# Kernel optimization log

Measured on AMD Instinct MI355X. Metric: run time of the kernel, lower is better.

## Reference

```python
import jax, jax.numpy as jnp
import numpy as np

TEMPERATURE = 0.2
EPS = 1e-8
N, D = 8192, 256
EDGE_PROB = 0.002  # ~16 neighbors per node


def setup_inputs() -> dict:
    key = jax.random.key(0)
    k1, k2, k3 = jax.random.split(key, 3)
    z_view = jax.random.normal(k1, (N, D), dtype=jnp.float32)
    z_fused = jax.random.normal(k2, (N, D), dtype=jnp.float32)
    # sparse binary fused-graph adjacency, densified (matches Gf_sparse.to_dense())
    Gf_dense = (jax.random.uniform(k3, (N, N)) < EDGE_PROB).astype(jnp.float32)
    return {"z_view": z_view, "z_fused": z_fused, "Gf_dense": Gf_dense}


def _l2_normalize(x, eps=1e-12):
    # matches F.normalize(p=2, dim=1): x / max(||x||, eps)
    norm = jnp.sqrt(jnp.sum(x * x, axis=1, keepdims=True))
    return x / jnp.maximum(norm, eps)


def reference(z_view, z_fused, Gf_dense):
    n = z_view.shape[0]
    zv = _l2_normalize(z_view)
    zf = _l2_normalize(z_fused)
    sim = jnp.matmul(zv, zf.T) / TEMPERATURE  # [N, N]
    eye = jnp.eye(n, dtype=sim.dtype)
    pos_mask = ((eye + Gf_dense) > 0).astype(sim.dtype)  # diag always 1
    neg_mask = 1.0 - pos_mask
    pos_scores = jnp.sum(sim * pos_mask, axis=1, keepdims=True) / (
        jnp.sum(pos_mask, axis=1, keepdims=True) + EPS
    )  # [N, 1]
    neg_scores = sim * neg_mask  # [N, N] (positive slots zeroed, kept as logits)
    logits = jnp.concatenate([pos_scores, neg_scores], axis=1)  # [N, N+1]
    # CrossEntropyLoss(reduction='sum') with labels == 0, then / N
    lse = jax.nn.logsumexp(logits, axis=1)
    loss = jnp.sum(lse - logits[:, 0]) / n
    return loss
```

## Files before the change

### kernel.cpp

```cpp
#include <hip/hip_runtime.h>

#define NROW 8192
#define DIM  256
#define INV_T 5.0f
#define BM 128
#define BN 128
#define CSPLIT 8
#define COLS_PER_BLOCK (NROW / CSPLIT)
#define NT (COLS_PER_BLOCK / BN)
#define TOTAL_STEPS (NT * (DIM / 32))

typedef _Float16 f16x8 __attribute__((ext_vector_type(8)));
typedef _Float16 f16x4 __attribute__((ext_vector_type(4)));
typedef float    f32x4 __attribute__((ext_vector_type(4)));

__device__ __forceinline__ void gload_lds16(const void* g, void* l) {
  __builtin_amdgcn_global_load_lds(
      (__attribute__((address_space(1))) void*)(g),
      (__attribute__((address_space(3))) void*)(l),
      16, 0, 0);
}

__global__ __launch_bounds__(256) void norm_kernel(
    const float* __restrict__ zv, const float* __restrict__ zf,
    _Float16* __restrict__ ov, _Float16* __restrict__ of) {
  const float* in  = blockIdx.y ? zf : zv;
  _Float16*    out = blockIdx.y ? of : ov;
  int row  = blockIdx.x * 4 + (threadIdx.x >> 6);
  int lane = threadIdx.x & 63;
  float4 v = ((const float4*)(in + (size_t)row * DIM))[lane];
  float ss = v.x * v.x + v.y * v.y + v.z * v.z + v.w * v.w;
#pragma unroll
  for (int off = 1; off < 64; off <<= 1) ss += __shfl_xor(ss, off);
  float inv = 1.0f / fmaxf(sqrtf(ss), 1e-12f);
  f16x4 o;
  o.x = (_Float16)(v.x * inv);
  o.y = (_Float16)(v.y * inv);
  o.z = (_Float16)(v.z * inv);
  o.w = (_Float16)(v.w * inv);
  ((f16x4*)(out + (size_t)row * DIM))[lane] = o;
}

__global__ __launch_bounds__(256, 2) void fused_kernel(
    const _Float16* __restrict__ zv, const _Float16* __restrict__ zf,
    const float* __restrict__ Gf,
    float* __restrict__ Sp, float* __restrict__ Pp, float* __restrict__ Cp) {

  __shared__ __align__(16) _Float16 Asf[BM * DIM];
  __shared__ __align__(16) _Float16 Bs[2][BN * 32];

  const int t    = threadIdx.x;
  const int lane = t & 63;
  const int w    = t >> 6;
  const int wr   = w >> 1;
  const int wc   = w & 1;
  const int l15  = lane & 15;
  const int kq   = lane >> 4;
  const int row0 = blockIdx.x * BM;
  const int col0 = blockIdx.y * COLS_PER_BLOCK;

#pragma unroll
  for (int c = 0; c < 16; ++c) {
    int i = c * 256 + t;
    int row = i >> 5, cbP = i & 31;
    int cbL = cbP ^ (row & 7);
    gload_lds16(zv + (size_t)(row0 + row) * DIM + cbL * 8,
                &Asf[(size_t)(c * 256 + w * 64) * 8]);
  }

  auto stageB = [&](int buf, int s) {
    int tt = s >> 3, kk = s & 7;
    int ct0 = col0 + tt * BN;
    int k0 = kk * 32;
#pragma unroll
    for (int c = 0; c < 2; ++c) {
      int i = c * 256 + t;
      int row = i >> 2, cbP = i & 3;
      int cbL = cbP ^ ((row >> 1) & 3);
      gload_lds16(zf + (size_t)(ct0 + row) * DIM + k0 + cbL * 8,
                  &Bs[buf][(size_t)(c * 256 + w * 64) * 8]);
    }
  };

  stageB(0, 0);
  asm volatile("s_waitcnt vmcnt(0)" ::: "memory");
  __syncthreads();

  f32x4 acc[4][4];
  float Sa[16], Pa[16], Ca[16];
#pragma unroll
  for (int i = 0; i < 16; ++i) { Sa[i] = 0.0f; Pa[i] = 0.0f; Ca[i] = 0.0f; }

#pragma unroll 2
  for (int s = 0; s < TOTAL_STEPS; ++s) {
    const int cur = s & 1;
    if ((s & 7) == 0) {
#pragma unroll
      for (int m = 0; m < 4; ++m)
#pragma unroll
        for (int n = 0; n < 4; ++n) acc[m][n] = (f32x4)(0.0f);
    }
    if (s < TOTAL_STEPS - 1) stageB(cur ^ 1, s + 1);

    const int k0 = (s & 7) * 32;
    f16x8 af[4], bf[4];
#pragma unroll
    for (int m = 0; m < 4; ++m) {
      int row = wr * 64 + m * 16 + l15;
      int cbL = (k0 >> 3) + kq;
      int cbP = cbL ^ (row & 7);
      af[m] = *(const f16x8*)&Asf[(size_t)row * 256 + cbP * 8];
    }
#pragma unroll
    for (int n = 0; n < 4; ++n) {
      int row = wc * 64 + n * 16 + l15;
      int cbP = kq ^ ((row >> 1) & 3);
      bf[n] = *(const f16x8*)&Bs[cur][(size_t)row * 32 + cbP * 8];
    }
#pragma unroll
    for (int m = 0; m < 4; ++m)
#pragma unroll
      for (int n = 0; n < 4; ++n)
        acc[m][n] = __builtin_amdgcn_mfma_f32_16x16x32_f16(af[m], bf[n], acc[m][n], 0, 0, 0);

    if ((s & 7) == 7) {
      int tt = s >> 3;
      int ct0 = col0 + tt * BN;
#pragma unroll
      for (int m = 0; m < 4; ++m) {
        int gi = row0 + wr * 64 + m * 16 + kq * 4;
#pragma unroll
        for (int n = 0; n < 4; ++n) {
          int gj = ct0 + wc * 64 + n * 16 + l15;
          const float* gp = Gf + (size_t)gi * NROW + gj;
#pragma unroll
          for (int r = 0; r < 4; ++r) {
            float sim = acc[m][n][r] * INV_T;
            float g = gp[(size_t)r * NROW];
            bool pos = (g > 0.0f) || ((gi + r) == gj);
            float e = __expf(sim);
            int idx = m * 4 + r;
            Sa[idx] += pos ? 1.0f : e;
            Pa[idx] += pos ? sim : 0.0f;
            Ca[idx] += pos ? 1.0f : 0.0f;
          }
        }
      }
    }
    asm volatile("s_waitcnt vmcnt(0)" ::: "memory");
    __syncthreads();
  }

#pragma unroll
  for (int off = 1; off <= 8; off <<= 1) {
#pragma unroll
    for (int i = 0; i < 16; ++i) {
      Sa[i] += __shfl_xor(Sa[i], off);
      Pa[i] += __shfl_xor(Pa[i], off);
      Ca[i] += __shfl_xor(Ca[i], off);
    }
  }
  const int slot = blockIdx.y * 2 + wc;
#pragma unroll
  for (int i = 0; i < 16; ++i) {
    if (l15 == i) {
      int m = i >> 2, r = i & 3;
      int row = row0 + wr * 64 + m * 16 + kq * 4 + r;
      Sp[(size_t)slot * NROW + row] = Sa[i];
      Pp[(size_t)slot * NROW + row] = Pa[i];
      Cp[(size_t)slot * NROW + row] = Ca[i];
    }
  }
}

__global__ __launch_bounds__(256) void loss_partial_kernel(
    const float* __restrict__ Sp, const float* __restrict__ Pp,
    const float* __restrict__ Cp, float* __restrict__ bsum) {
  int row = blockIdx.x * 256 + threadIdx.x;
  float S = 0.0f, P = 0.0f, C = 0.0f;
#pragma unroll
  for (int s2 = 0; s2 < 16; ++s2) {
    S += Sp[(size_t)s2 * NROW + row];
    P += Pp[(size_t)s2 * NROW + row];
    C += Cp[(size_t)s2 * NROW + row];
  }
  float pos = P / (C + 1e-8f);
  float contrib = __logf(S + __expf(pos)) - pos;
#pragma unroll
  for (int off = 1; off < 64; off <<= 1) contrib += __shfl_xor(contrib, off);
  __shared__ float wsum[4];
  if ((threadIdx.x & 63) == 0) wsum[threadIdx.x >> 6] = contrib;
  __syncthreads();
  if (threadIdx.x == 0) bsum[blockIdx.x] = wsum[0] + wsum[1] + wsum[2] + wsum[3];
}

__global__ void loss_final_kernel(const float* __restrict__ bsum, float* __restrict__ out) {
  int lane = threadIdx.x;
  float v = (lane < 32) ? bsum[lane] : 0.0f;
#pragma unroll
  for (int off = 1; off < 64; off <<= 1) v += __shfl_xor(v, off);
  if (lane == 0) out[0] = v / (float)NROW;
}

extern "C" void kernel_launch(void* const* d_in, const int* in_sizes, int n_in,
                              void* d_out, int out_size, void* d_ws, size_t ws_size,
                              hipStream_t stream) {
  const float* zv = (const float*)d_in[0];
  const float* zf = (const float*)d_in[1];
  const float* Gf = (const float*)d_in[2];
  float* out = (float*)d_out;

  char* ws = (char*)d_ws;
  _Float16* zv16 = (_Float16*)ws;
  _Float16* zf16 = zv16 + (size_t)NROW * DIM;
  float* Sp = (float*)(ws + 2 * (size_t)NROW * DIM * sizeof(_Float16));
  float* Pp = Sp + 16 * (size_t)NROW;
  float* Cp = Pp + 16 * (size_t)NROW;
  float* bsum = Cp + 16 * (size_t)NROW;

  norm_kernel<<<dim3(NROW / 4, 2), 256, 0, stream>>>(zv, zf, zv16, zf16);
  fused_kernel<<<dim3(NROW / BM, CSPLIT), 256, 0, stream>>>(zv16, zf16, Gf, Sp, Pp, Cp);
  loss_partial_kernel<<<NROW / 256, 256, 0, stream>>>(Sp, Pp, Cp, bsum);
  loss_final_kernel<<<1, 64, 0, stream>>>(bsum, out);
}
```

Baseline: 113.4 us.

## Prefetch adjacency tiles as float4 into ballot bitmasks overlapped with MFMA steps

Replaces the per-element scalar Gf loads in the epilogue with vectorized float4 loads of the next column tile's adjacency, issued during the K-steps of the current tile and packed into per-wave 64-bit masks via ballots. The epilogue then tests bits instead of waiting on global loads. The K loop is fully unrolled per tile with fine-grained vmcnt waits and raw s_barrier in place of __syncthreads. This is meant to hide the latency of the scattered Gf reads behind compute, at the cost of more registers and more complex wait-count bookkeeping.

Result: faster. 102.6 us (-9.5%).

```diff
diff --git a/kernel.cpp b/kernel.cpp
--- a/kernel.cpp
+++ b/kernel.cpp
@@ -7,12 +7,12 @@
 #define BN 128
 #define CSPLIT 8
 #define COLS_PER_BLOCK (NROW / CSPLIT)
-#define NT (COLS_PER_BLOCK / BN)
-#define TOTAL_STEPS (NT * (DIM / 32))
+#define NT 8
 
 typedef _Float16 f16x8 __attribute__((ext_vector_type(8)));
 typedef _Float16 f16x4 __attribute__((ext_vector_type(4)));
 typedef float    f32x4 __attribute__((ext_vector_type(4)));
+typedef unsigned long long u64;
 
 __device__ __forceinline__ void gload_lds16(const void* g, void* l) {
   __builtin_amdgcn_global_load_lds(
@@ -49,9 +49,9 @@
   __shared__ __align__(16) _Float16 Asf[BM * DIM];
   __shared__ __align__(16) _Float16 Bs[2][BN * 32];
 
-  const int t    = threadIdx.x;
-  const int lane = t & 63;
-  const int w    = t >> 6;
+  const int t_   = threadIdx.x;
+  const int lane = t_ & 63;
+  const int w    = t_ >> 6;
   const int wr   = w >> 1;
   const int wc   = w & 1;
   const int l15  = lane & 15;
@@ -61,7 +61,7 @@
 
 #pragma unroll
   for (int c = 0; c < 16; ++c) {
-    int i = c * 256 + t;
+    int i = c * 256 + t_;
     int row = i >> 5, cbP = i & 31;
     int cbL = cbP ^ (row & 7);
     gload_lds16(zv + (size_t)(row0 + row) * DIM + cbL * 8,
@@ -74,7 +74,7 @@
     int k0 = kk * 32;
 #pragma unroll
     for (int c = 0; c < 2; ++c) {
-      int i = c * 256 + t;
+      int i = c * 256 + t_;
       int row = i >> 2, cbP = i & 3;
       int cbL = cbP ^ ((row >> 1) & 3);
       gload_lds16(zf + (size_t)(ct0 + row) * DIM + k0 + cbL * 8,
@@ -82,74 +82,126 @@
     }
   };
 
+  auto issueGf = [&](float4* q, int tt, int c0) {
+    const float* base = Gf + (size_t)(row0 + wr * 64 + (lane >> 4)) * NROW
+                           + col0 + tt * BN + wc * 64 + l15 * 4;
+#pragma unroll
+    for (int j = 0; j < 4; ++j)
+      q[j] = *(const float4*)(base + (size_t)((c0 + j) * 4) * NROW);
+  };
+
+  auto maskFrom4 = [&](const float4* q) -> u64 {
+    u64 e = 0;
+#pragma unroll
+    for (int j = 0; j < 4; ++j) {
+      u64 b0 = __ballot(q[j].x > 0.0f);
+      u64 b1 = __ballot(q[j].y > 0.0f);
+      u64 b2 = __ballot(q[j].z > 0.0f);
+      u64 b3 = __ballot(q[j].w > 0.0f);
+      u64 s01 = (l15 & 1) ? b1 : b0;
+      u64 s23 = (l15 & 1) ? b3 : b2;
+      u64 bsel = (l15 & 2) ? s23 : s01;
+      u64 ej = bsel >> (l15 >> 2);
+      e = (kq == j) ? ej : e;
+    }
+    return e;
+  };
+
   stageB(0, 0);
+
+  u64 wm[4];
+  {
+    float4 gp[8];
+#pragma unroll
+    for (int c = 0; c < 8; ++c) issueGf(gp + c, 0, c);
+    wm[0] = maskFrom4(gp);
+    wm[1] = maskFrom4(gp + 4);
+#pragma unroll
+    for (int c = 0; c < 8; ++c) issueGf(gp + c, 0, 8 + c);
+    wm[2] = maskFrom4(gp);
+    wm[3] = maskFrom4(gp + 4);
+  }
   asm volatile("s_waitcnt vmcnt(0)" ::: "memory");
-  __syncthreads();
+  __builtin_amdgcn_s_barrier();
 
   f32x4 acc[4][4];
   float Sa[16], Pa[16], Ca[16];
+  u64 wn[4];
+  float4 gvA[4], gvB[4];
 #pragma unroll
   for (int i = 0; i < 16; ++i) { Sa[i] = 0.0f; Pa[i] = 0.0f; Ca[i] = 0.0f; }
 
-#pragma unroll 2
-  for (int s = 0; s < TOTAL_STEPS; ++s) {
-    const int cur = s & 1;
-    if ((s & 7) == 0) {
-#pragma unroll
-      for (int m = 0; m < 4; ++m)
-#pragma unroll
-        for (int n = 0; n < 4; ++n) acc[m][n] = (f32x4)(0.0f);
-    }
-    if (s < TOTAL_STEPS - 1) stageB(cur ^ 1, s + 1);
-
-    const int k0 = (s & 7) * 32;
-    f16x8 af[4], bf[4];
-#pragma unroll
-    for (int m = 0; m < 4; ++m) {
-      int row = wr * 64 + m * 16 + l15;
-      int cbL = (k0 >> 3) + kq;
-      int cbP = cbL ^ (row & 7);
-      af[m] = *(const f16x8*)&Asf[(size_t)row * 256 + cbP * 8];
-    }
-#pragma unroll
-    for (int n = 0; n < 4; ++n) {
-      int row = wc * 64 + n * 16 + l15;
-      int cbP = kq ^ ((row >> 1) & 3);
-      bf[n] = *(const f16x8*)&Bs[cur][(size_t)row * 32 + cbP * 8];
-    }
-#pragma unroll
-    for (int m = 0; m < 4; ++m)
-#pragma unroll
-      for (int n = 0; n < 4; ++n)
-        acc[m][n] = __builtin_amdgcn_mfma_f32_16x16x32_f16(af[m], bf[n], acc[m][n], 0, 0, 0);
-
-    if ((s & 7) == 7) {
-      int tt = s >> 3;
-      int ct0 = col0 + tt * BN;
-#pragma unroll
-      for (int m = 0; m < 4; ++m) {
-        int gi = row0 + wr * 64 + m * 16 + kq * 4;
-#pragma unroll
-        for (int n = 0; n < 4; ++n) {
-          int gj = ct0 + wc * 64 + n * 16 + l15;
-          const float* gp = Gf + (size_t)gi * NROW + gj;
-#pragma unroll
-          for (int r = 0; r < 4; ++r) {
-            float sim = acc[m][n][r] * INV_T;
-            float g = gp[(size_t)r * NROW];
-            bool pos = (g > 0.0f) || ((gi + r) == gj);
-            float e = __expf(sim);
-            int idx = m * 4 + r;
-            Sa[idx] += pos ? 1.0f : e;
-            Pa[idx] += pos ? sim : 0.0f;
-            Ca[idx] += pos ? 1.0f : 0.0f;
-          }
-        }
-      }
-    }
-    asm volatile("s_waitcnt vmcnt(0)" ::: "memory");
-    __syncthreads();
-  }
+#define STEP(KK)                                                               \
+  do {                                                                         \
+    if ((KK) == 0) {                                                           \
+      _Pragma("unroll") for (int m = 0; m < 4; ++m)                            \
+          _Pragma("unroll") for (int n = 0; n < 4; ++n)                        \
+              acc[m][n] = (f32x4)(0.0f);                                       \
+    }                                                                          \
+    f16x8 af[4], bf[4];                                                        \
+    _Pragma("unroll") for (int m = 0; m < 4; ++m) {                            \
+      int row = wr * 64 + m * 16 + l15;                                        \
+      int cbL = ((KK) * 32 >> 3) + kq;                                         \
+      int cbP = cbL ^ (row & 7);                                               \
+      af[m] = *(const f16x8*)&Asf[(size_t)row * 256 + cbP * 8];                \
+    }                                                                          \
+    _Pragma("unroll") for (int n = 0; n < 4; ++n) {                            \
+      int row = wc * 64 + n * 16 + l15;                                        \
+      int cbP = kq ^ ((row >> 1) & 3);                                         \
+      bf[n] = *(const f16x8*)&Bs[(KK) & 1][(size_t)row * 32 + cbP * 8];        \
+    }                                                                          \
+    if (t < NT - 1 || (KK) < 7) stageB(((KK) + 1) & 1, t * 8 + (KK) + 1);      \
+    asm volatile("" ::: "memory");                                             \
+    if ((KK) < 4) {                                                            \
+      if (t < NT - 1) issueGf(((KK) & 1) ? gvB : gvA, t + 1, (KK) * 4);        \
+    }                                                                          \
+    asm volatile("" ::: "memory");                                             \
+    _Pragma("unroll") for (int m = 0; m < 4; ++m)                              \
+        _Pragma("unroll") for (int n = 0; n < 4; ++n)                          \
+            acc[m][n] = __builtin_amdgcn_mfma_f32_16x16x32_f16(                \
+                af[m], bf[n], acc[m][n], 0, 0, 0);                             \
+    if ((KK) >= 1 && (KK) <= 4) {                                              \
+      if (t < NT - 1) wn[(KK) - 1] = maskFrom4(((KK) & 1) ? gvA : gvB);        \
+    }                                                                          \
+    if ((KK) == 7) {                                                           \
+      int ct0 = col0 + t * BN;                                                 \
+      _Pragma("unroll") for (int m = 0; m < 4; ++m) {                          \
+        int gi = row0 + wr * 64 + m * 16 + kq * 4;                             \
+        _Pragma("unroll") for (int n = 0; n < 4; ++n) {                        \
+          int gj = ct0 + wc * 64 + n * 16 + l15;                               \
+          _Pragma("unroll") for (int r = 0; r < 4; ++r) {                      \
+            float sim = acc[m][n][r] * INV_T;                                  \
+            bool pos = (((unsigned)(wm[m] >> (r * 16 + n * 4)) & 1u) != 0u) || \
+                       ((gi + r) == gj);                                       \
+            float e = __expf(sim);                                             \
+            int idx = m * 4 + r;                                               \
+            Sa[idx] += pos ? 1.0f : e;                                         \
+            Pa[idx] += pos ? sim : 0.0f;                                       \
+            Ca[idx] += pos ? 1.0f : 0.0f;                                      \
+          }                                                                    \
+        }                                                                      \
+      }                                                                        \
+      if (t < NT - 1) {                                                        \
+        _Pragma("unroll") for (int i = 0; i < 4; ++i) wm[i] = wn[i];           \
+      }                                                                        \
+    }                                                                          \
+    if ((KK) < 4) {                                                            \
+      if (t < NT - 1)                                                          \
+        asm volatile("s_waitcnt vmcnt(4)" ::: "memory");                       \
+      else                                                                     \
+        asm volatile("s_waitcnt vmcnt(0)" ::: "memory");                       \
+    } else {                                                                   \
+      asm volatile("s_waitcnt vmcnt(0)" ::: "memory");                         \
+    }                                                                          \
+    __builtin_amdgcn_s_barrier();                                              \
+  } while (0)
+
+#pragma unroll 1
+  for (int t = 0; t < NT; ++t) {
+    STEP(0); STEP(1); STEP(2); STEP(3);
+    STEP(4); STEP(5); STEP(6); STEP(7);
+  }
+#undef STEP
 
 #pragma unroll
   for (int off = 1; off <= 8; off <<= 1) {
```

## Split dense GEMM exp-sum from sparse positive-edge correction into heterogeneous blocks

Applied to the files above, without the earlier changes.

The GEMM blocks now only accumulate exp(sim) over all columns and no longer read the adjacency matrix in their epilogue. A second kind of block in the same grid streams Gf rows, finds positive entries with a wave ballot, and recomputes those few similarities with a dot product to collect positive sum, count and exp for correction. The final reduction forms S = E - sE + C. This takes the 256MB Gf read out of the MFMA-bound blocks' epilogue and overlaps it with GEMM blocks, at the cost of a few redundant sparse dot products and slight numeric differences from subtracting exp terms.

New measurement: 208.0 us. +83.5%, slower.

```diff
diff --git a/kernel.cpp b/kernel.cpp
--- a/kernel.cpp
+++ b/kernel.cpp
@@ -7,12 +7,12 @@
 #define BN 128
 #define CSPLIT 8
 #define COLS_PER_BLOCK (NROW / CSPLIT)
-#define NT (COLS_PER_BLOCK / BN)
-#define TOTAL_STEPS (NT * (DIM / 32))
+#define NT 8
 
 typedef _Float16 f16x8 __attribute__((ext_vector_type(8)));
 typedef _Float16 f16x4 __attribute__((ext_vector_type(4)));
 typedef float    f32x4 __attribute__((ext_vector_type(4)));
+typedef unsigned long long u64;
 
 __device__ __forceinline__ void gload_lds16(const void* g, void* l) {
   __builtin_amdgcn_global_load_lds(
@@ -41,149 +41,207 @@
   ((f16x4*)(out + (size_t)row * DIM))[lane] = o;
 }
 
-__global__ __launch_bounds__(256, 2) void fused_kernel(
+__global__ __launch_bounds__(256, 2) void main_kernel(
     const _Float16* __restrict__ zv, const _Float16* __restrict__ zf,
     const float* __restrict__ Gf,
-    float* __restrict__ Sp, float* __restrict__ Pp, float* __restrict__ Cp) {
+    float* __restrict__ Ep, float* __restrict__ Pp,
+    float* __restrict__ sEp, float* __restrict__ Cp) {
 
   __shared__ __align__(16) _Float16 Asf[BM * DIM];
   __shared__ __align__(16) _Float16 Bs[2][BN * 32];
 
-  const int t    = threadIdx.x;
-  const int lane = t & 63;
-  const int w    = t >> 6;
-  const int wr   = w >> 1;
-  const int wc   = w & 1;
-  const int l15  = lane & 15;
-  const int kq   = lane >> 4;
-  const int row0 = blockIdx.x * BM;
-  const int col0 = blockIdx.y * COLS_PER_BLOCK;
-
-#pragma unroll
-  for (int c = 0; c < 16; ++c) {
-    int i = c * 256 + t;
-    int row = i >> 5, cbP = i & 31;
-    int cbL = cbP ^ (row & 7);
-    gload_lds16(zv + (size_t)(row0 + row) * DIM + cbL * 8,
-                &Asf[(size_t)(c * 256 + w * 64) * 8]);
-  }
-
-  auto stageB = [&](int buf, int s) {
-    int tt = s >> 3, kk = s & 7;
-    int ct0 = col0 + tt * BN;
-    int k0 = kk * 32;
-#pragma unroll
-    for (int c = 0; c < 2; ++c) {
-      int i = c * 256 + t;
-      int row = i >> 2, cbP = i & 3;
-      int cbL = cbP ^ ((row >> 1) & 3);
-      gload_lds16(zf + (size_t)(ct0 + row) * DIM + k0 + cbL * 8,
-                  &Bs[buf][(size_t)(c * 256 + w * 64) * 8]);
-    }
-  };
-
-  stageB(0, 0);
-  asm volatile("s_waitcnt vmcnt(0)" ::: "memory");
-  __syncthreads();
-
-  f32x4 acc[4][4];
-  float Sa[16], Pa[16], Ca[16];
-#pragma unroll
-  for (int i = 0; i < 16; ++i) { Sa[i] = 0.0f; Pa[i] = 0.0f; Ca[i] = 0.0f; }
+  const int bid  = blockIdx.x;
+  const int cb   = bid & 7;
+  const int kind = (bid >> 3) & 1;
+  const int rb   = bid >> 4;
+  const int t_   = threadIdx.x;
+  const int lane = t_ & 63;
+  const int row0 = rb * BM;
+  const int col0 = cb * COLS_PER_BLOCK;
+
+  if (kind == 0) {
+    const int w   = t_ >> 6;
+    const int wr  = w >> 1;
+    const int wc  = w & 1;
+    const int l15 = lane & 15;
+    const int kq  = lane >> 4;
+
+#pragma unroll
+    for (int c = 0; c < 16; ++c) {
+      int i = c * 256 + t_;
+      int row = i >> 5, cbP = i & 31;
+      int cbL = cbP ^ (row & 7);
+      gload_lds16(zv + (size_t)(row0 + row) * DIM + cbL * 8,
+                  &Asf[(size_t)(c * 256 + w * 64) * 8]);
+    }
+
+    auto stageB = [&](int buf, int s) {
+      int tt = s >> 3, kk = s & 7;
+      int ct0 = col0 + tt * BN;
+      int k0 = kk * 32;
+#pragma unroll
+      for (int c = 0; c < 2; ++c) {
+        int i = c * 256 + t_;
+        int row = i >> 2, cbP = i & 3;
+        int cbL = cbP ^ ((row >> 1) & 3);
+        gload_lds16(zf + (size_t)(ct0 + row) * DIM + k0 + cbL * 8,
+                    &Bs[buf][(size_t)(c * 256 + w * 64) * 8]);
+      }
+    };
+
+    stageB(0, 0);
+    asm volatile("s_waitcnt vmcnt(0)" ::: "memory");
+    __syncthreads();
+
+    f32x4 acc[4][4];
+    float Sa[16];
+#pragma unroll
+    for (int i = 0; i < 16; ++i) Sa[i] = 0.0f;
 
 #pragma unroll 2
-  for (int s = 0; s < TOTAL_STEPS; ++s) {
-    const int cur = s & 1;
-    if ((s & 7) == 0) {
+    for (int s = 0; s < 64; ++s) {
+      const int cur = s & 1;
+      if ((s & 7) == 0) {
+#pragma unroll
+        for (int m = 0; m < 4; ++m)
+#pragma unroll
+          for (int n = 0; n < 4; ++n) acc[m][n] = (f32x4)(0.0f);
+      }
+      if (s < 63) stageB(cur ^ 1, s + 1);
+
+      const int k0 = (s & 7) * 32;
+      f16x8 af[4], bf[4];
+#pragma unroll
+      for (int m = 0; m < 4; ++m) {
+        int row = wr * 64 + m * 16 + l15;
+        int cbL = (k0 >> 3) + kq;
+        int cbP = cbL ^ (row & 7);
+        af[m] = *(const f16x8*)&Asf[(size_t)row * 256 + cbP * 8];
+      }
+#pragma unroll
+      for (int n = 0; n < 4; ++n) {
+        int row = wc * 64 + n * 16 + l15;
+        int cbP = kq ^ ((row >> 1) & 3);
+        bf[n] = *(const f16x8*)&Bs[cur][(size_t)row * 32 + cbP * 8];
+      }
 #pragma unroll
       for (int m = 0; m < 4; ++m)
 #pragma unroll
-        for (int n = 0; n < 4; ++n) acc[m][n] = (f32x4)(0.0f);
-    }
-    if (s < TOTAL_STEPS - 1) stageB(cur ^ 1, s + 1);
-
-    const int k0 = (s & 7) * 32;
-    f16x8 af[4], bf[4];
-#pragma unroll
-    for (int m = 0; m < 4; ++m) {
-      int row = wr * 64 + m * 16 + l15;
-      int cbL = (k0 >> 3) + kq;
-      int cbP = cbL ^ (row & 7);
-      af[m] = *(const f16x8*)&Asf[(size_t)row * 256 + cbP * 8];
-    }
-#pragma unroll
-    for (int n = 0; n < 4; ++n) {
-      int row = wc * 64 + n * 16 + l15;
-      int cbP = kq ^ ((row >> 1) & 3);
-      bf[n] = *(const f16x8*)&Bs[cur][(size_t)row * 32 + cbP * 8];
-    }
-#pragma unroll
-    for (int m = 0; m < 4; ++m)
-#pragma unroll
-      for (int n = 0; n < 4; ++n)
-        acc[m][n] = __builtin_amdgcn_mfma_f32_16x16x32_f16(af[m], bf[n], acc[m][n], 0, 0, 0);
-
-    if ((s & 7) == 7) {
-      int tt = s >> 3;
-      int ct0 = col0 + tt * BN;
-#pragma unroll
-      for (int m = 0; m < 4; ++m) {
-        int gi = row0 + wr * 64 + m * 16 + kq * 4;
-#pragma unroll
-        for (int n = 0; n < 4; ++n) {
-          int gj = ct0 + wc * 64 + n * 16 + l15;
-          const float* gp = Gf + (size_t)gi * NROW + gj;
-#pragma unroll
-          for (int r = 0; r < 4; ++r) {
-            float sim = acc[m][n][r] * INV_T;
-            float g = gp[(size_t)r * NROW];
-            bool pos = (g > 0.0f) || ((gi + r) == gj);
-            float e = __expf(sim);
-            int idx = m * 4 + r;
-            Sa[idx] += pos ? 1.0f : e;
-            Pa[idx] += pos ? sim : 0.0f;
-            Ca[idx] += pos ? 1.0f : 0.0f;
+        for (int n = 0; n < 4; ++n)
+          acc[m][n] = __builtin_amdgcn_mfma_f32_16x16x32_f16(af[m], bf[n], acc[m][n], 0, 0, 0);
+
+      if ((s & 7) == 7) {
+#pragma unroll
+        for (int m = 0; m < 4; ++m)
+#pragma unroll
+          for (int n = 0; n < 4; ++n)
+#pragma unroll
+            for (int r = 0; r < 4; ++r)
+              Sa[m * 4 + r] += __expf(acc[m][n][r] * INV_T);
+      }
+      asm volatile("s_waitcnt vmcnt(0)" ::: "memory");
+      __builtin_amdgcn_s_barrier();
+    }
+
+#pragma unroll
+    for (int off = 1; off <= 8; off <<= 1)
+#pragma unroll
+      for (int i = 0; i < 16; ++i) Sa[i] += __shfl_xor(Sa[i], off);
+
+    const int slot = cb * 2 + wc;
+#pragma unroll
+    for (int i = 0; i < 16; ++i) {
+      if (l15 == i) {
+        int m = i >> 2, r = i & 3;
+        int row = row0 + wr * 64 + m * 16 + kq * 4 + r;
+        Ep[(size_t)slot * NROW + row] = Sa[i];
+      }
+    }
+  } else {
+    const int wv = t_ >> 6;
+    const int rowbase = row0 + wv * 32;
+
+    float4 bufA[4], bufB[4];
+    const float* gbase = Gf + (size_t)rowbase * NROW + col0 + lane * 4;
+
+    auto issueRow = [&](float4* q, int r) {
+      const float* p = gbase + (size_t)r * NROW;
+#pragma unroll
+      for (int c = 0; c < 4; ++c) q[c] = *(const float4*)(p + c * 256);
+    };
+
+    auto procRow = [&](const float4* q, int r) {
+      const int i = rowbase + r;
+      f16x4 a16 = *(const f16x4*)(zv + (size_t)i * DIM + lane * 4);
+      float a0 = (float)a16[0], a1 = (float)a16[1], a2 = (float)a16[2], a3 = (float)a16[3];
+      float P = 0.0f, E = 0.0f, C = 0.0f;
+#pragma unroll
+      for (int c = 0; c < 4; ++c) {
+        float4 qq = q[c];
+        int j0 = col0 + lane * 4 + c * 256;
+        bool any = (qq.x > 0.0f) | (qq.y > 0.0f) | (qq.z > 0.0f) | (qq.w > 0.0f);
+        bool dg = ((unsigned)(i - j0)) < 4u;
+        u64 b = __ballot(any || dg);
+        while (b) {
+          int L = (int)__builtin_ctzll(b);
+          b &= b - 1;
+          float g0 = __shfl(qq.x, L), g1 = __shfl(qq.y, L);
+          float g2 = __shfl(qq.z, L), g3 = __shfl(qq.w, L);
+          int j0L = col0 + L * 4 + c * 256;
+#pragma unroll
+          for (int cc = 0; cc < 4; ++cc) {
+            float g = (cc == 0) ? g0 : (cc == 1) ? g1 : (cc == 2) ? g2 : g3;
+            int jj = j0L + cc;
+            if (g > 0.0f || jj == i) {
+              f16x4 b16 = *(const f16x4*)(zf + (size_t)jj * DIM + lane * 4);
+              float d = a0 * (float)b16[0] + a1 * (float)b16[1] +
+                        a2 * (float)b16[2] + a3 * (float)b16[3];
+#pragma unroll
+              for (int off = 1; off < 64; off <<= 1) d += __shfl_xor(d, off);
+              float sim = d * INV_T;
+              P += sim;
+              E += __expf(sim);
+              C += 1.0f;
+            }
           }
         }
       }
-    }
-    asm volatile("s_waitcnt vmcnt(0)" ::: "memory");
-    __syncthreads();
+      if (lane == 0) {
+        Pp [(size_t)cb * NROW + i] = P;
+        sEp[(size_t)cb * NROW + i] = E;
+        Cp [(size_t)cb * NROW + i] = C;
+      }
+    };
+
+    issueRow(bufA, 0);
+    asm volatile("" ::: "memory");
+#pragma unroll 1
+    for (int r = 0; r < 32; r += 2) {
+      if (r + 1 < 32) issueRow(bufB, r + 1);
+      asm volatile("" ::: "memory");
+      procRow(bufA, r);
+      if (r + 2 < 32) issueRow(bufA, r + 2);
+      asm volatile("" ::: "memory");
+      if (r + 1 < 32) procRow(bufB, r + 1);
+    }
   }
-
-#pragma unroll
-  for (int off = 1; off <= 8; off <<= 1) {
-#pragma unroll
-    for (int i = 0; i < 16; ++i) {
-      Sa[i] += __shfl_xor(Sa[i], off);
-      Pa[i] += __shfl_xor(Pa[i], off);
-      Ca[i] += __shfl_xor(Ca[i], off);
-    }
+}
+
+__global__ __launch_bounds__(256) void loss_partial_kernel(
+    const float* __restrict__ Ep, const float* __restrict__ Pp,
+    const float* __restrict__ sEp, const float* __restrict__ Cp,
+    float* __restrict__ bsum) {
+  int row = blockIdx.x * 256 + threadIdx.x;
+  float E = 0.0f, P = 0.0f, sE = 0.0f, C = 0.0f;
+#pragma unroll
+  for (int s2 = 0; s2 < 16; ++s2) E += Ep[(size_t)s2 * NROW + row];
+#pragma unroll
+  for (int s2 = 0; s2 < 8; ++s2) {
+    P  += Pp [(size_t)s2 * NROW + row];
+    sE += sEp[(size_t)s2 * NROW + row];
+    C  += Cp [(size_t)s2 * NROW + row];
   }
-  const int slot = blockIdx.y * 2 + wc;
-#pragma unroll
-  for (int i = 0; i < 16; ++i) {
-    if (l15 == i) {
-      int m = i >> 2, r = i & 3;
-      int row = row0 + wr * 64 + m * 16 + kq * 4 + r;
-      Sp[(size_t)slot * NROW + row] = Sa[i];
-      Pp[(size_t)slot * NROW + row] = Pa[i];
-      Cp[(size_t)slot * NROW + row] = Ca[i];
-    }
-  }
-}
-
-__global__ __launch_bounds__(256) void loss_partial_kernel(
-    const float* __restrict__ Sp, const float* __restrict__ Pp,
-    const float* __restrict__ Cp, float* __restrict__ bsum) {
-  int row = blockIdx.x * 256 + threadIdx.x;
-  float S = 0.0f, P = 0.0f, C = 0.0f;
-#pragma unroll
-  for (int s2 = 0; s2 < 16; ++s2) {
-    S += Sp[(size_t)s2 * NROW + row];
-    P += Pp[(size_t)s2 * NROW + row];
-    C += Cp[(size_t)s2 * NROW + row];
-  }
+  float S = E - sE + C;
   float pos = P / (C + 1e-8f);
   float contrib = __logf(S + __expf(pos)) - pos;
 #pragma unroll
@@ -213,13 +271,14 @@
   char* ws = (char*)d_ws;
   _Float16* zv16 = (_Float16*)ws;
   _Float16* zf16 = zv16 + (size_t)NROW * DIM;
-  float* Sp = (float*)(ws + 2 * (size_t)NROW * DIM * sizeof(_Float16));
-  float* Pp = Sp + 16 * (size_t)NROW;
-  float* Cp = Pp + 16 * (size_t)NROW;
-  float* bsum = Cp + 16 * (size_t)NROW;
+  float* Ep  = (float*)(ws + 2 * (size_t)NROW * DIM * sizeof(_Float16));
+  float* Pp  = Ep  + 16 * (size_t)NROW;
+  float* sEp = Pp  + 8 * (size_t)NROW;
+  float* Cp  = sEp + 8 * (size_t)NROW;
+  float* bsum = Cp + 8 * (size_t)NROW;
 
   norm_kernel<<<dim3(NROW / 4, 2), 256, 0, stream>>>(zv, zf, zv16, zf16);
-  fused_kernel<<<dim3(NROW / BM, CSPLIT), 256, 0, stream>>>(zv16, zf16, Gf, Sp, Pp, Cp);
-  loss_partial_kernel<<<NROW / 256, 256, 0, stream>>>(Sp, Pp, Cp, bsum);
+  main_kernel<<<1024, 256, 0, stream>>>(zv16, zf16, Gf, Ep, Pp, sEp, Cp);
+  loss_partial_kernel<<<NROW / 256, 256, 0, stream>>>(Ep, Pp, sEp, Cp, bsum);
   loss_final_kernel<<<1, 64, 0, stream>>>(bsum, out);
 }
```
